# Optimization experiments

Measured on AMD Instinct MI355X. Metric: run time of the kernel, lower is better.

Reference implementation:

```python
import jax, jax.numpy as jnp
import numpy as np

NHEAD = 4
DIM = 256

def rotate_half(x):
    # interleaved: out[..., ::2] = -x[..., 1::2]; out[..., 1::2] = x[..., ::2]
    xe = x[..., ::2]
    xo = x[..., 1::2]
    return jnp.stack([-xo, xe], axis=-1).reshape(x.shape)

def rope_2d(q, k, H, W):
    Dh = q.shape[-1]
    half = Dh // 2
    inv_freq = 1.0 / (10000.0 ** (jnp.arange(half, dtype=jnp.float32) / half))  # [half]
    yy, xx = jnp.meshgrid(jnp.arange(H, dtype=jnp.float32), jnp.arange(W, dtype=jnp.float32), indexing='ij')
    ang_y = yy.reshape(-1)[:, None] * inv_freq  # [N, half]
    ang_x = xx.reshape(-1)[:, None] * inv_freq  # [N, half]
    cy, sy = jnp.cos(ang_y), jnp.sin(ang_y)
    cx, sx = jnp.cos(ang_x), jnp.sin(ang_x)
    def rot(t):
        t1 = t[..., :half]          # y-rotated half
        t2 = t[..., half:2 * half]  # x-rotated half
        ty = t1 * cy + rotate_half(t1) * sy
        tx = t2 * cx + rotate_half(t2) * sx
        return jnp.concatenate([ty, tx, t[..., 2 * half:]], axis=-1)
    return rot(q), rot(k)

def layernorm(x, g, b, eps=1e-5):
    mu = jnp.mean(x, axis=-1, keepdims=True)
    var = jnp.var(x, axis=-1, keepdims=True)
    return (x - mu) / jnp.sqrt(var + eps) * g + b

def setup_inputs() -> dict:
    key = jax.random.key(0)
    ks = jax.random.split(key, 8)
    B, Hs, Ws, C = 4, 48, 48, DIM
    N = Hs * Ws
    s = 0.02
    return {
        'x': jax.random.normal(ks[0], (B, N, C), dtype=jnp.float32),
        'Wqkv': jax.random.normal(ks[1], (3 * C, C), dtype=jnp.float32) * s,
        'Wproj': jax.random.normal(ks[2], (C, C), dtype=jnp.float32) * s,
        'g1': jnp.ones((C,), jnp.float32), 'b1': jnp.zeros((C,), jnp.float32),
        'g2': jnp.ones((C,), jnp.float32), 'b2': jnp.zeros((C,), jnp.float32),
        'W1': jax.random.normal(ks[3], (4 * C, C), dtype=jnp.float32) * s,
        'bf1': jnp.zeros((4 * C,), jnp.float32),
        'W2': jax.random.normal(ks[4], (C, 4 * C), dtype=jnp.float32) * s,
        'bf2': jnp.zeros((C,), jnp.float32),
        'H': Hs, 'W': Ws,
    }

def reference(x, Wqkv, Wproj, g1, b1, g2, b2, W1, bf1, W2, bf2, H, W):
    B, N, C = x.shape
    dh = C // NHEAD
    qkv = (x @ Wqkv.T).reshape(B, N, 3, NHEAD, dh).transpose(2, 0, 3, 1, 4)  # [3,B,h,N,dh]
    q, k, v = qkv[0], qkv[1], qkv[2]
    q, k = rope_2d(q, k, H, W)
    scores = jnp.einsum('bhnd,bhmd->bhnm', q, k) / jnp.sqrt(jnp.float32(dh))
    attn = jax.nn.softmax(scores, axis=-1)  # drop_attn is identity (p=0)
    out = jnp.einsum('bhnm,bhmd->bhnd', attn, v).transpose(0, 2, 1, 3).reshape(B, N, C)
    x = x + out @ Wproj.T
    x = layernorm(x, g1, b1)
    h = jax.nn.gelu(x @ W1.T + bf1, approximate=False)
    x = x + h @ W2.T + bf2
    return layernorm(x, g2, b2)
```

## Files before the change

### kernel.cpp

```cpp
#include <hip/hip_runtime.h>
#include <hip/hip_bf16.h>
#include <math.h>

typedef __hip_bfloat16 bf16;
typedef __attribute__((ext_vector_type(8))) short short8;
typedef __attribute__((ext_vector_type(4))) short short4v;
typedef __attribute__((ext_vector_type(4))) float f32x4;

#define NSEQ 2304
#define CDIM 256
#define NHD  4
#define DH   64

#if __has_builtin(__builtin_amdgcn_exp2f)
#define EXP2F __builtin_amdgcn_exp2f
#else
#define EXP2F exp2f
#endif

static __device__ __forceinline__ f32x4 mfma_bf16(short8 a, short8 b, f32x4 c) {
  return __builtin_amdgcn_mfma_f32_16x16x32_bf16(a, b, c, 0, 0, 0);
}
static __device__ __forceinline__ short8 ld8(const bf16* p) {
  return *reinterpret_cast<const short8*>(p);
}
static __device__ __forceinline__ short8 lds8(const bf16* p) {
  return *reinterpret_cast<const short8*>(p);
}
static __device__ __forceinline__ float b2f(short v) {
  unsigned int u = ((unsigned int)(unsigned short)v) << 16;
  return __uint_as_float(u);
}
static __device__ __forceinline__ short f2b(float f) {
  bf16 h = __float2bfloat16(f);
  return *reinterpret_cast<short*>(&h);
}

__global__ __launch_bounds__(256) void detect_kernel(const void* __restrict__ xraw,
                                                     int* __restrict__ flag) {
  int t = threadIdx.x;
  const unsigned short* s = (const unsigned short*)xraw;
  int bad = 0;
#pragma unroll
  for (int i = 0; i < 8; ++i) {
    unsigned idx = (((unsigned)(t * 8 + i)) * 9173u) & ((1u << 20) - 1);
    unsigned short v = s[idx * 2];
    unsigned e = (v >> 7) & 0xFFu;
    if (e > 133u) bad++;
  }
  __shared__ int tot;
  if (t == 0) tot = 0;
  __syncthreads();
  atomicAdd(&tot, bad);
  __syncthreads();
  if (t == 0) flag[0] = (tot >= 16) ? 1 : 0;
}

__global__ __launch_bounds__(256) void cvt_all_kernel(const void* sx, const void* sqkv, const void* sproj,
                                                      const void* sw1, const void* sw2,
                                                      const void* g1, const void* b1, const void* g2,
                                                      const void* b2, const void* bias1, const void* bias2,
                                                      bf16* dx, bf16* dqkv, bf16* dproj,
                                                      bf16* dw1, bf16* dw2, bf16* dsm,
                                                      const int* __restrict__ flag) {
  int is32 = flag[0];
  int bid = blockIdx.x;
  const void* src; bf16* dst; int i4;
  if (bid < 2304)      { src = sx;    dst = dx;    i4 = bid * 256 + threadIdx.x; }
  else if (bid < 2496) { src = sqkv;  dst = dqkv;  i4 = (bid - 2304) * 256 + threadIdx.x; }
  else if (bid < 2560) { src = sproj; dst = dproj; i4 = (bid - 2496) * 256 + threadIdx.x; }
  else if (bid < 2816) { src = sw1;   dst = dw1;   i4 = (bid - 2560) * 256 + threadIdx.x; }
  else if (bid < 3072) { src = sw2;   dst = dw2;   i4 = (bid - 2816) * 256 + threadIdx.x; }
  else {
    const void* srcs[6] = {g1, b1, g2, b2, bias1, bias2};
    const int ns[6] = {256, 256, 256, 256, 1024, 256};
    const int off[6] = {0, 256, 512, 768, 1024, 2048};
    int t = threadIdx.x;
#pragma unroll
    for (int j = 0; j < 6; ++j)
      for (int i = t; i < ns[j]; i += 256) {
        if (is32) dsm[off[j] + i] = __float2bfloat16(((const float*)srcs[j])[i]);
        else      dsm[off[j] + i] = ((const bf16*)srcs[j])[i];
      }
    return;
  }
  if (is32) {
    float4 v = ((const float4*)src)[i4];
    short4v o;
    o[0] = f2b(v.x); o[1] = f2b(v.y); o[2] = f2b(v.z); o[3] = f2b(v.w);
    ((short4v*)dst)[i4] = o;
  } else {
    ((short4v*)dst)[i4] = ((const short4v*)src)[i4];
  }
}

__global__ __launch_bounds__(256, 1) void qkv_kernel(const bf16* __restrict__ X,
                                                     const bf16* __restrict__ Wqkv,
                                                     bf16* __restrict__ Q, bf16* __restrict__ K,
                                                     bf16* __restrict__ Vt,
                                                     const int* __restrict__ Wp) {
  int wave = threadIdx.x >> 6, lane = threadIdx.x & 63;
  int l15 = lane & 15, quad = lane >> 4;
  int m0 = (blockIdx.x * 4 + wave) * 64;
  int n0 = blockIdx.y * 64;
  const bf16* arow = X + (size_t)(m0 + l15) * CDIM + quad * 8;
  const bf16* brow = Wqkv + (size_t)(n0 + l15) * CDIM + quad * 8;
  f32x4 z = {0.f, 0.f, 0.f, 0.f};
  f32x4 acc[4][4];
#pragma unroll
  for (int j = 0; j < 4; ++j)
#pragma unroll
    for (int i = 0; i < 4; ++i) acc[j][i] = z;

  short8 a[4], b[4];
#pragma unroll
  for (int i = 0; i < 4; ++i) a[i] = ld8(arow + (size_t)i * 16 * CDIM);
#pragma unroll
  for (int j = 0; j < 4; ++j) b[j] = ld8(brow + (size_t)j * 16 * CDIM);
#pragma unroll
  for (int kk = 32; kk <= CDIM; kk += 32) {
    short8 an[4], bn[4];
    if (kk < CDIM) {
#pragma unroll
      for (int i = 0; i < 4; ++i) an[i] = ld8(arow + (size_t)i * 16 * CDIM + kk);
#pragma unroll
      for (int j = 0; j < 4; ++j) bn[j] = ld8(brow + (size_t)j * 16 * CDIM + kk);
    }
#pragma unroll
    for (int j = 0; j < 4; ++j)
#pragma unroll
      for (int i = 0; i < 4; ++i) acc[j][i] = mfma_bf16(b[j], a[i], acc[j][i]);
    if (kk < CDIM) {
#pragma unroll
      for (int i = 0; i < 4; ++i) a[i] = an[i];
#pragma unroll
      for (int j = 0; j < 4; ++j) b[j] = bn[j];
    }
  }

  int which = n0 >> 8, h = (n0 & 255) >> 6;
  if (which == 2) {
#pragma unroll
    for (int j = 0; j < 4; ++j) {
      int d0 = j * 16 + quad * 4;
#pragma unroll
      for (int i = 0; i < 4; ++i) {
        int gm = m0 + i * 16 + l15;
        int bb = gm / NSEQ, n = gm % NSEQ;
        int bh = bb * NHD + h;
#pragma unroll
        for (int r = 0; r < 4; ++r)
          Vt[((size_t)bh * DH + d0 + r) * NSEQ + n] = __float2bfloat16(acc[j][i][r]);
      }
    }
  } else {
    int Wv = Wp[0];
    if (Wv <= 0 || Wv > 65536) Wv = 48;
    bf16* dst = (which == 0) ? Q : K;
    const float cc = -0.28782313662425574f;
    const float EC1 = 0.7498942434f, EC2 = 0.5623413252f, EC3 = 0.4216965034f;
#pragma unroll
    for (int i = 0; i < 4; ++i) {
      int gm = m0 + i * 16 + l15;
      int bb = gm / NSEQ, n = gm % NSEQ;
      int bh = bb * NHD + h;
      int py = n / Wv, px = n - py * Wv;
#pragma unroll
      for (int j = 0; j < 4; ++j) {
        int d0 = j * 16 + quad * 4;
        float pos = (d0 & 32) ? (float)px : (float)py;
        int base = d0 & 31;
        float fb = __expf(cc * (float)base);
        float f0 = fb, f1 = fb * EC1, f2 = fb * EC2, f3 = fb * EC3;
        float s0, c0, s1, c1, s2, c2, s3, c3;
        __sincosf(pos * f0, &s0, &c0);
        __sincosf(pos * f1, &s1, &c1);
        __sincosf(pos * f2, &s2, &c2);
        __sincosf(pos * f3, &s3, &c3);
        float a0 = acc[j][i][0], a1 = acc[j][i][1], a2 = acc[j][i][2], a3 = acc[j][i][3];
        short4v ov;
        ov[0] = f2b(a0 * c0 - a1 * s0);
        ov[1] = f2b(a1 * c1 + a0 * s1);
        ov[2] = f2b(a2 * c2 - a3 * s2);
        ov[3] = f2b(a3 * c3 + a2 * s3);
        *reinterpret_cast<short4v*>(dst + ((size_t)bh * NSEQ + n) * DH + d0) = ov;
      }
    }
  }
}

__global__ __launch_bounds__(128, 2) void attn_kernel(const bf16* __restrict__ Q, const bf16* __restrict__ K,
                                                      const bf16* __restrict__ Vt, bf16* __restrict__ AO) {
  int bh = blockIdx.x, qt = blockIdx.y;
  int tid = threadIdx.x;
  int wave = tid >> 6, lane = tid & 63;
  int l15 = lane & 15, quad = lane >> 4;
  int m0 = qt * 64 + wave * 32;
  const bf16* Qb = Q + (size_t)bh * NSEQ * DH;
  const bf16* Kb = K + (size_t)bh * NSEQ * DH;
  const bf16* Vb = Vt + (size_t)bh * DH * NSEQ;

  __shared__ __align__(16) bf16 kbuf[2][64 * 72];
  __shared__ __align__(16) bf16 vbuf[2][64 * 72];
  __shared__ __align__(16) bf16 plds[2][32 * 72];

  int rs[4], cs[4];
#pragma unroll
  for (int j = 0; j < 4; ++j) {
    int i = tid + j * 128;
    rs[j] = i >> 3;
    cs[j] = (i & 7) * 8;
  }

  const float QS = 0.18033688011112042f;
  short8 qa0 = ld8(Qb + (size_t)(m0 + l15) * DH + quad * 8);
  short8 qa1 = ld8(Qb + (size_t)(m0 + l15) * DH + 32 + quad * 8);
  short8 qb0 = ld8(Qb + (size_t)(m0 + 16 + l15) * DH + quad * 8);
  short8 qb1 = ld8(Qb + (size_t)(m0 + 16 + l15) * DH + 32 + quad * 8);
#pragma unroll
  for (int i = 0; i < 8; ++i) {
    qa0[i] = f2b(b2f(qa0[i]) * QS);
    qa1[i] = f2b(b2f(qa1[i]) * QS);
    qb0[i] = f2b(b2f(qb0[i]) * QS);
    qb1[i] = f2b(b2f(qb1[i]) * QS);
  }

  f32x4 z = {0.f, 0.f, 0.f, 0.f};
  f32x4 o[4] = {z, z, z, z};
  f32x4 o2[4] = {z, z, z, z};
  float l_run = 0.f, l_run2 = 0.f;
  bf16* pb = plds[wave];

#pragma unroll
  for (int j = 0; j < 4; ++j) {
    *reinterpret_cast<short8*>(kbuf[0] + rs[j] * 72 + cs[j]) = ld8(Kb + (size_t)rs[j] * DH + cs[j]);
    *reinterpret_cast<short8*>(vbuf[0] + rs[j] * 72 + cs[j]) = ld8(Vb + (size_t)rs[j] * NSEQ + cs[j]);
  }
  __syncthreads();

  for (int it = 0; it < NSEQ / 64; ++it) {
    int cur = it & 1;
    bool more = (it + 1 < NSEQ / 64);

    short8 kpre[4], vpre[4];
    if (more) {
      int kn = (it + 1) * 64;
#pragma unroll
      for (int j = 0; j < 4; ++j) {
        kpre[j] = ld8(Kb + (size_t)(kn + rs[j]) * DH + cs[j]);
        vpre[j] = ld8(Vb + (size_t)rs[j] * NSEQ + kn + cs[j]);
      }
    }

    const bf16* kb = kbuf[cur];
    const bf16* vb = vbuf[cur];

    f32x4 s[4], s2[4];
#pragma unroll
    for (int kt = 0; kt < 4; ++kt) {
      const bf16* kp = kb + (size_t)(kt * 16 + l15) * 72 + quad * 8;
      short8 kf0 = lds8(kp);
      short8 kf1 = lds8(kp + 32);
      s[kt] = mfma_bf16(kf0, qa0, z);
      s[kt] = mfma_bf16(kf1, qa1, s[kt]);
      s2[kt] = mfma_bf16(kf0, qb0, z);
      s2[kt] = mfma_bf16(kf1, qb1, s2[kt]);
    }

    float ls = 0.f, ls2 = 0.f;
#pragma unroll
    for (int kt = 0; kt < 4; ++kt) {
      float p0 = EXP2F(s[kt][0]);
      float p1 = EXP2F(s[kt][1]);
      float p2 = EXP2F(s[kt][2]);
      float p3 = EXP2F(s[kt][3]);
      ls += (p0 + p1) + (p2 + p3);
      short4v pk;
      pk[0] = f2b(p0); pk[1] = f2b(p1); pk[2] = f2b(p2); pk[3] = f2b(p3);
      *reinterpret_cast<short4v*>(pb + l15 * 72 + kt * 16 + quad * 4) = pk;
      float q0 = EXP2F(s2[kt][0]);
      float q1 = EXP2F(s2[kt][1]);
      float q2 = EXP2F(s2[kt][2]);
      float q3 = EXP2F(s2[kt][3]);
      ls2 += (q0 + q1) + (q2 + q3);
      short4v pk2;
      pk2[0] = f2b(q0); pk2[1] = f2b(q1); pk2[2] = f2b(q2); pk2[3] = f2b(q3);
      *reinterpret_cast<short4v*>(pb + (16 + l15) * 72 + kt * 16 + quad * 4) = pk2;
    }
    l_run += ls;
    l_run2 += ls2;

#pragma unroll
    for (int kt2 = 0; kt2 < 2; ++kt2) {
      short8 pfA = lds8(pb + l15 * 72 + kt2 * 32 + quad * 8);
      short8 pfB = lds8(pb + (16 + l15) * 72 + kt2 * 32 + quad * 8);
#pragma unroll
      for (int t = 0; t < 4; ++t) {
        short8 vf = lds8(vb + (size_t)(t * 16 + l15) * 72 + kt2 * 32 + quad * 8);
        o[t] = mfma_bf16(vf, pfA, o[t]);
        o2[t] = mfma_bf16(vf, pfB, o2[t]);
      }
    }

    if (more) {
      bf16* kn_ = kbuf[1 - cur];
      bf16* vn_ = vbuf[1 - cur];
#pragma unroll
      for (int j = 0; j < 4; ++j) {
        *reinterpret_cast<short8*>(kn_ + rs[j] * 72 + cs[j]) = kpre[j];
        *reinterpret_cast<short8*>(vn_ + rs[j] * 72 + cs[j]) = vpre[j];
      }
    }
    __syncthreads();
  }

  l_run += __shfl_xor(l_run, 16);
  l_run += __shfl_xor(l_run, 32);
  l_run2 += __shfl_xor(l_run2, 16);
  l_run2 += __shfl_xor(l_run2, 32);
  float inv = 1.f / l_run;
  float inv2 = 1.f / l_run2;
  int b = bh >> 2, h = bh & 3;
  bf16* orow = AO + ((size_t)b * NSEQ + (m0 + l15)) * CDIM + h * DH;
  bf16* orow2 = AO + ((size_t)b * NSEQ + (m0 + 16 + l15)) * CDIM + h * DH;
#pragma unroll
  for (int t = 0; t < 4; ++t) {
    short4v ov, ov2;
#pragma unroll
    for (int r = 0; r < 4; ++r) {
      ov[r] = f2b(o[t][r] * inv);
      ov2[r] = f2b(o2[t][r] * inv2);
    }
    *reinterpret_cast<short4v*>(orow + t * 16 + quad * 4) = ov;
    *reinterpret_cast<short4v*>(orow2 + t * 16 + quad * 4) = ov2;
  }
}

template <int KD, int EPI, int TI>
__global__ __launch_bounds__(256) void gemm128(const bf16* __restrict__ A, const bf16* __restrict__ Wm,
                                               const bf16* __restrict__ bias, const bf16* __restrict__ res,
                                               bf16* __restrict__ outp, int NC) {
  constexpr int KS = KD / 32;
  constexpr int AR = TI * 32;
  int tid = threadIdx.x;
  int wave = tid >> 6, lane = tid & 63;
  int l15 = lane & 15, quad = lane >> 4;
  int wm = (wave >> 1) * (TI * 16);
  int wn = (wave & 1) * 64;
  int m0 = blockIdx.x * AR;
  int n0 = blockIdx.y * 128;

  __shared__ __align__(16) bf16 abuf[2][AR * 40];
  __shared__ __align__(16) bf16 bbuf[2][128 * 40];

  int sr = tid >> 2, sc = (tid & 3) * 8;

  const bf16* ag[TI / 2];
#pragma unroll
  for (int u = 0; u < TI / 2; ++u) ag[u] = A + (size_t)(m0 + sr + u * 64) * KD + sc;
  const bf16* bg0 = Wm + (size_t)(n0 + sr) * KD + sc;
  const bf16* bg1 = Wm + (size_t)(n0 + 64 + sr) * KD + sc;

  f32x4 z = {0.f, 0.f, 0.f, 0.f};
  f32x4 acc[4][TI];
#pragma unroll
  for (int j = 0; j < 4; ++j)
#pragma unroll
    for (int i = 0; i < TI; ++i) acc[j][i] = z;

#pragma unroll
  for (int u = 0; u < TI / 2; ++u)
    *reinterpret_cast<short8*>(abuf[0] + (sr + u * 64) * 40 + sc) = ld8(ag[u]);
  *reinterpret_cast<short8*>(bbuf[0] + sr * 40 + sc) = ld8(bg0);
  *reinterpret_cast<short8*>(bbuf[0] + (64 + sr) * 40 + sc) = ld8(bg1);
  __syncthreads();

  for (int s = 0; s < KS; ++s) {
    int cur = s & 1;
    bool more = (s + 1 < KS);
    short8 anx[TI / 2], bnx0, bnx1;
    if (more) {
#pragma unroll
      for (int u = 0; u < TI / 2; ++u) anx[u] = ld8(ag[u] + (s + 1) * 32);
      bnx0 = ld8(bg0 + (s + 1) * 32);
      bnx1 = ld8(bg1 + (s + 1) * 32);
    }
    short8 af[TI], bf_[4];
#pragma unroll
    for (int i = 0; i < TI; ++i)
      af[i] = lds8(abuf[cur] + (size_t)(wm + i * 16 + l15) * 40 + quad * 8);
#pragma unroll
    for (int j = 0; j < 4; ++j)
      bf_[j] = lds8(bbuf[cur] + (size_t)(wn + j * 16 + l15) * 40 + quad * 8);
#pragma unroll
    for (int j = 0; j < 4; ++j)
#pragma unroll
      for (int i = 0; i < TI; ++i)
        acc[j][i] = mfma_bf16(bf_[j], af[i], acc[j][i]);
    if (more) {
#pragma unroll
      for (int u = 0; u < TI / 2; ++u)
        *reinterpret_cast<short8*>(abuf[1 - cur] + (sr + u * 64) * 40 + sc) = anx[u];
      *reinterpret_cast<short8*>(bbuf[1 - cur] + sr * 40 + sc) = bnx0;
      *reinterpret_cast<short8*>(bbuf[1 - cur] + (64 + sr) * 40 + sc) = bnx1;
    }
    __syncthreads();
  }

#pragma unroll
  for (int j = 0; j < 4; ++j) {
    int col0 = n0 + wn + j * 16 + quad * 4;
    float bb4[4];
    if (EPI != 0) {
      short4v bl = *reinterpret_cast<const short4v*>(bias + col0);
#pragma unroll
      for (int r = 0; r < 4; ++r) bb4[r] = b2f(bl[r]);
    }
#pragma unroll
    for (int i = 0; i < TI; ++i) {
      size_t idx = (size_t)(m0 + wm + i * 16 + l15) * NC + col0;
      short4v ov;
      if (EPI == 0) {
        short4v rl = *reinterpret_cast<const short4v*>(res + idx);
#pragma unroll
        for (int r = 0; r < 4; ++r) ov[r] = f2b(acc[j][i][r] + b2f(rl[r]));
      } else if (EPI == 1) {
#pragma unroll
        for (int r = 0; r < 4; ++r) {
          float hv = acc[j][i][r] + bb4[r];
          ov[r] = f2b(0.5f * hv * (1.f + erff(hv * 0.70710678118f)));
        }
      } else {
        short4v rl = *reinterpret_cast<const short4v*>(res + idx);
#pragma unroll
        for (int r = 0; r < 4; ++r) ov[r] = f2b(acc[j][i][r] + bb4[r] + b2f(rl[r]));
      }
      *reinterpret_cast<short4v*>(outp + idx) = ov;
    }
  }
}

__global__ __launch_bounds__(256) void ln_kernel(const bf16* __restrict__ X, const bf16* __restrict__ g,
                                                 const bf16* __restrict__ bv, bf16* __restrict__ out) {
  int row = blockIdx.x * 4 + (threadIdx.x >> 6);
  int lane = threadIdx.x & 63;
  short4v raw = *reinterpret_cast<const short4v*>(X + (size_t)row * CDIM + lane * 4);
  float vv[4];
  float s = 0.f, sq = 0.f;
#pragma unroll
  for (int i = 0; i < 4; ++i) {
    float f = b2f(raw[i]);
    vv[i] = f; s += f; sq += f * f;
  }
#pragma unroll
  for (int off = 1; off < 64; off <<= 1) { s += __shfl_xor(s, off); sq += __shfl_xor(sq, off); }
  float mu = s * (1.f / CDIM);
  float var = sq * (1.f / CDIM) - mu * mu;
  float rstd = rsqrtf(var + 1e-5f);
#pragma unroll
  for (int i = 0; i < 4; ++i) {
    int c = lane * 4 + i;
    out[(size_t)row * CDIM + c] =
        __float2bfloat16((vv[i] - mu) * rstd * __bfloat162float(g[c]) + __bfloat162float(bv[c]));
  }
}

__global__ __launch_bounds__(256) void ln_out_kernel(const bf16* __restrict__ X, const bf16* __restrict__ g,
                                                     const bf16* __restrict__ bv, void* __restrict__ out,
                                                     const int* __restrict__ flag) {
  int is32 = flag[0];
  int row = blockIdx.x * 4 + (threadIdx.x >> 6);
  int lane = threadIdx.x & 63;
  short4v raw = *reinterpret_cast<const short4v*>(X + (size_t)row * CDIM + lane * 4);
  float vv[4];
  float s = 0.f, sq = 0.f;
#pragma unroll
  for (int i = 0; i < 4; ++i) {
    float f = b2f(raw[i]);
    vv[i] = f; s += f; sq += f * f;
  }
#pragma unroll
  for (int off = 1; off < 64; off <<= 1) { s += __shfl_xor(s, off); sq += __shfl_xor(sq, off); }
  float mu = s * (1.f / CDIM);
  float var = sq * (1.f / CDIM) - mu * mu;
  float rstd = rsqrtf(var + 1e-5f);
#pragma unroll
  for (int i = 0; i < 4; ++i) {
    int c = lane * 4 + i;
    size_t idx = (size_t)row * CDIM + c;
    float v = (vv[i] - mu) * rstd * __bfloat162float(g[c]) + __bfloat162float(bv[c]);
    if (is32) ((float*)out)[idx] = v;
    else      ((bf16*)out)[idx] = __float2bfloat16(v);
  }
}

extern "C" void kernel_launch(void* const* d_in, const int* in_sizes, int n_in,
                              void* d_out, int out_size, void* d_ws, size_t ws_size,
                              hipStream_t stream) {
  const int* Wp = (const int*)d_in[12];

  char* ws = (char*)d_ws;
  const size_t SZ = 4718592;
  bf16* Qc  = (bf16*)(ws + 0 * SZ);
  bf16* Kc  = (bf16*)(ws + 1 * SZ);
  bf16* Vt  = (bf16*)(ws + 2 * SZ);
  bf16* AO  = (bf16*)(ws + 3 * SZ);
  bf16* F   = (bf16*)(ws + 4 * SZ);
  bf16* Y   = (bf16*)(ws + 5 * SZ);
  bf16* xc  = (bf16*)(ws + 6 * SZ);
  bf16* G   = (bf16*)(ws + 0);
  bf16* Wqkvc  = (bf16*)(ws + 7 * SZ);
  bf16* Wprojc = (bf16*)(ws + 7 * SZ + 393216);
  bf16* W1c    = (bf16*)(ws + 7 * SZ + 524288);
  bf16* W2c    = (bf16*)(ws + 7 * SZ + 1048576);
  bf16* smallc = (bf16*)(ws + 7 * SZ + 1572864);
  bf16* g1c  = smallc + 0;
  bf16* b1c  = smallc + 256;
  bf16* g2c  = smallc + 512;
  bf16* b2c  = smallc + 768;
  bf16* bf1c = smallc + 1024;
  bf16* bf2c = smallc + 2048;
  int*  flagp = (int*)(ws + 7 * SZ + 1581568);
  bf16* outsc = (bf16*)d_out;

  detect_kernel<<<1, 256, 0, stream>>>(d_in[0], flagp);
  cvt_all_kernel<<<3073, 256, 0, stream>>>(d_in[0], d_in[1], d_in[2], d_in[7], d_in[9],
                                           d_in[3], d_in[4], d_in[5], d_in[6], d_in[8], d_in[10],
                                           xc, Wqkvc, Wprojc, W1c, W2c, smallc, flagp);

  qkv_kernel<<<dim3(36, 12), 256, 0, stream>>>(xc, Wqkvc, Qc, Kc, Vt, Wp);
  attn_kernel<<<dim3(16, 36), 128, 0, stream>>>(Qc, Kc, Vt, AO);
  gemm128<256, 0, 2><<<dim3(144, 2), 256, 0, stream>>>(AO, Wprojc, nullptr, xc, outsc, 256);
  ln_kernel<<<2304, 256, 0, stream>>>(outsc, g1c, b1c, F);
  gemm128<256, 1, 4><<<dim3(72, 8), 256, 0, stream>>>(F, W1c, bf1c, nullptr, G, 1024);
  gemm128<1024, 2, 2><<<dim3(144, 2), 256, 0, stream>>>(G, W2c, bf2c, F, Y, 256);
  ln_out_kernel<<<2304, 256, 0, stream>>>(Y, g2c, b2c, d_out, flagp);
}
```

Baseline: 217.7 us.

## Split attention key tiles across two wave pairs with LDS reduction

The attention block grows from 2 to 4 waves. Each pair of waves takes half of every 64-key tile, which halves per-wave MFMA and exp work per iteration. Partial outputs and row sums are combined through LDS, reusing the K buffer, at the end. This raises wave-level parallelism for the 576 blocks at the cost of an extra reduction step and more threads contending at each barrier.

Result: faster. 212.4 us (-2.5%).

```diff
diff --git a/kernel.cpp b/kernel.cpp
--- a/kernel.cpp
+++ b/kernel.cpp
@@ -189,28 +189,25 @@
   }
 }
 
-__global__ __launch_bounds__(128, 2) void attn_kernel(const bf16* __restrict__ Q, const bf16* __restrict__ K,
+__global__ __launch_bounds__(256, 3) void attn_kernel(const bf16* __restrict__ Q, const bf16* __restrict__ K,
                                                       const bf16* __restrict__ Vt, bf16* __restrict__ AO) {
   int bh = blockIdx.x, qt = blockIdx.y;
   int tid = threadIdx.x;
   int wave = tid >> 6, lane = tid & 63;
   int l15 = lane & 15, quad = lane >> 4;
-  int m0 = qt * 64 + wave * 32;
+  int qf = wave & 1;
+  int ks = wave >> 1;
+  int m0 = qt * 64 + qf * 32;
   const bf16* Qb = Q + (size_t)bh * NSEQ * DH;
   const bf16* Kb = K + (size_t)bh * NSEQ * DH;
   const bf16* Vb = Vt + (size_t)bh * DH * NSEQ;
 
   __shared__ __align__(16) bf16 kbuf[2][64 * 72];
   __shared__ __align__(16) bf16 vbuf[2][64 * 72];
-  __shared__ __align__(16) bf16 plds[2][32 * 72];
-
-  int rs[4], cs[4];
-#pragma unroll
-  for (int j = 0; j < 4; ++j) {
-    int i = tid + j * 128;
-    rs[j] = i >> 3;
-    cs[j] = (i & 7) * 8;
-  }
+  __shared__ __align__(16) bf16 plds[4][32 * 40];
+
+  int r1 = tid >> 3, c1 = (tid & 7) * 8;
+  int r1b = r1 + 32;
 
   const float QS = 0.18033688011112042f;
   short8 qa0 = ld8(Qb + (size_t)(m0 + l15) * DH + quad * 8);
@@ -231,34 +228,32 @@
   float l_run = 0.f, l_run2 = 0.f;
   bf16* pb = plds[wave];
 
-#pragma unroll
-  for (int j = 0; j < 4; ++j) {
-    *reinterpret_cast<short8*>(kbuf[0] + rs[j] * 72 + cs[j]) = ld8(Kb + (size_t)rs[j] * DH + cs[j]);
-    *reinterpret_cast<short8*>(vbuf[0] + rs[j] * 72 + cs[j]) = ld8(Vb + (size_t)rs[j] * NSEQ + cs[j]);
-  }
+  *reinterpret_cast<short8*>(kbuf[0] + r1 * 72 + c1)  = ld8(Kb + (size_t)r1 * DH + c1);
+  *reinterpret_cast<short8*>(kbuf[0] + r1b * 72 + c1) = ld8(Kb + (size_t)r1b * DH + c1);
+  *reinterpret_cast<short8*>(vbuf[0] + r1 * 72 + c1)  = ld8(Vb + (size_t)r1 * NSEQ + c1);
+  *reinterpret_cast<short8*>(vbuf[0] + r1b * 72 + c1) = ld8(Vb + (size_t)r1b * NSEQ + c1);
   __syncthreads();
 
   for (int it = 0; it < NSEQ / 64; ++it) {
     int cur = it & 1;
     bool more = (it + 1 < NSEQ / 64);
 
-    short8 kpre[4], vpre[4];
+    short8 kpA, kpB, vpA, vpB;
     if (more) {
       int kn = (it + 1) * 64;
-#pragma unroll
-      for (int j = 0; j < 4; ++j) {
-        kpre[j] = ld8(Kb + (size_t)(kn + rs[j]) * DH + cs[j]);
-        vpre[j] = ld8(Vb + (size_t)rs[j] * NSEQ + kn + cs[j]);
-      }
+      kpA = ld8(Kb + (size_t)(kn + r1) * DH + c1);
+      kpB = ld8(Kb + (size_t)(kn + r1b) * DH + c1);
+      vpA = ld8(Vb + (size_t)r1 * NSEQ + kn + c1);
+      vpB = ld8(Vb + (size_t)r1b * NSEQ + kn + c1);
     }
 
     const bf16* kb = kbuf[cur];
     const bf16* vb = vbuf[cur];
 
-    f32x4 s[4], s2[4];
-#pragma unroll
-    for (int kt = 0; kt < 4; ++kt) {
-      const bf16* kp = kb + (size_t)(kt * 16 + l15) * 72 + quad * 8;
+    f32x4 s[2], s2[2];
+#pragma unroll
+    for (int kt = 0; kt < 2; ++kt) {
+      const bf16* kp = kb + (size_t)(ks * 32 + kt * 16 + l15) * 72 + quad * 8;
       short8 kf0 = lds8(kp);
       short8 kf1 = lds8(kp + 32);
       s[kt] = mfma_bf16(kf0, qa0, z);
@@ -269,7 +264,7 @@
 
     float ls = 0.f, ls2 = 0.f;
 #pragma unroll
-    for (int kt = 0; kt < 4; ++kt) {
+    for (int kt = 0; kt < 2; ++kt) {
       float p0 = EXP2F(s[kt][0]);
       float p1 = EXP2F(s[kt][1]);
       float p2 = EXP2F(s[kt][2]);
@@ -277,7 +272,7 @@
       ls += (p0 + p1) + (p2 + p3);
       short4v pk;
       pk[0] = f2b(p0); pk[1] = f2b(p1); pk[2] = f2b(p2); pk[3] = f2b(p3);
-      *reinterpret_cast<short4v*>(pb + l15 * 72 + kt * 16 + quad * 4) = pk;
+      *reinterpret_cast<short4v*>(pb + l15 * 40 + kt * 16 + quad * 4) = pk;
       float q0 = EXP2F(s2[kt][0]);
       float q1 = EXP2F(s2[kt][1]);
       float q2 = EXP2F(s2[kt][2]);
@@ -285,18 +280,17 @@
       ls2 += (q0 + q1) + (q2 + q3);
       short4v pk2;
       pk2[0] = f2b(q0); pk2[1] = f2b(q1); pk2[2] = f2b(q2); pk2[3] = f2b(q3);
-      *reinterpret_cast<short4v*>(pb + (16 + l15) * 72 + kt * 16 + quad * 4) = pk2;
+      *reinterpret_cast<short4v*>(pb + (16 + l15) * 40 + kt * 16 + quad * 4) = pk2;
     }
     l_run += ls;
     l_run2 += ls2;
 
-#pragma unroll
-    for (int kt2 = 0; kt2 < 2; ++kt2) {
-      short8 pfA = lds8(pb + l15 * 72 + kt2 * 32 + quad * 8);
-      short8 pfB = lds8(pb + (16 + l15) * 72 + kt2 * 32 + quad * 8);
+    {
+      short8 pfA = lds8(pb + l15 * 40 + quad * 8);
+      short8 pfB = lds8(pb + (16 + l15) * 40 + quad * 8);
 #pragma unroll
       for (int t = 0; t < 4; ++t) {
-        short8 vf = lds8(vb + (size_t)(t * 16 + l15) * 72 + kt2 * 32 + quad * 8);
+        short8 vf = lds8(vb + (size_t)(t * 16 + l15) * 72 + ks * 32 + quad * 8);
         o[t] = mfma_bf16(vf, pfA, o[t]);
         o2[t] = mfma_bf16(vf, pfB, o2[t]);
       }
@@ -305,34 +299,62 @@
     if (more) {
       bf16* kn_ = kbuf[1 - cur];
       bf16* vn_ = vbuf[1 - cur];
-#pragma unroll
-      for (int j = 0; j < 4; ++j) {
-        *reinterpret_cast<short8*>(kn_ + rs[j] * 72 + cs[j]) = kpre[j];
-        *reinterpret_cast<short8*>(vn_ + rs[j] * 72 + cs[j]) = vpre[j];
-      }
+      *reinterpret_cast<short8*>(kn_ + r1 * 72 + c1)  = kpA;
+      *reinterpret_cast<short8*>(kn_ + r1b * 72 + c1) = kpB;
+      *reinterpret_cast<short8*>(vn_ + r1 * 72 + c1)  = vpA;
+      *reinterpret_cast<short8*>(vn_ + r1b * 72 + c1) = vpB;
     }
     __syncthreads();
   }
 
-  l_run += __shfl_xor(l_run, 16);
-  l_run += __shfl_xor(l_run, 32);
-  l_run2 += __shfl_xor(l_run2, 16);
-  l_run2 += __shfl_xor(l_run2, 32);
-  float inv = 1.f / l_run;
-  float inv2 = 1.f / l_run2;
-  int b = bh >> 2, h = bh & 3;
-  bf16* orow = AO + ((size_t)b * NSEQ + (m0 + l15)) * CDIM + h * DH;
-  bf16* orow2 = AO + ((size_t)b * NSEQ + (m0 + 16 + l15)) * CDIM + h * DH;
-#pragma unroll
-  for (int t = 0; t < 4; ++t) {
-    short4v ov, ov2;
-#pragma unroll
-    for (int r = 0; r < 4; ++r) {
-      ov[r] = f2b(o[t][r] * inv);
-      ov2[r] = f2b(o2[t][r] * inv2);
-    }
-    *reinterpret_cast<short4v*>(orow + t * 16 + quad * 4) = ov;
-    *reinterpret_cast<short4v*>(orow2 + t * 16 + quad * 4) = ov2;
+  float* scr = (float*)kbuf;
+  int slot = qf * 64 + lane;
+  if (ks == 1) {
+    float* p = scr + slot * 36;
+#pragma unroll
+    for (int t = 0; t < 4; ++t) {
+      *reinterpret_cast<f32x4*>(p + t * 4) = o[t];
+      *reinterpret_cast<f32x4*>(p + 16 + t * 4) = o2[t];
+    }
+    p[32] = l_run;
+    p[33] = l_run2;
+  }
+  __syncthreads();
+  if (ks == 0) {
+    float* p = scr + slot * 36;
+#pragma unroll
+    for (int t = 0; t < 4; ++t) {
+      f32x4 pa = *reinterpret_cast<f32x4*>(p + t * 4);
+      f32x4 pb2 = *reinterpret_cast<f32x4*>(p + 16 + t * 4);
+#pragma unroll
+      for (int r = 0; r < 4; ++r) {
+        o[t][r] += pa[r];
+        o2[t][r] += pb2[r];
+      }
+    }
+    l_run += p[32];
+    l_run2 += p[33];
+
+    l_run += __shfl_xor(l_run, 16);
+    l_run += __shfl_xor(l_run, 32);
+    l_run2 += __shfl_xor(l_run2, 16);
+    l_run2 += __shfl_xor(l_run2, 32);
+    float inv = 1.f / l_run;
+    float inv2 = 1.f / l_run2;
+    int b = bh >> 2, h = bh & 3;
+    bf16* orow = AO + ((size_t)b * NSEQ + (m0 + l15)) * CDIM + h * DH;
+    bf16* orow2 = AO + ((size_t)b * NSEQ + (m0 + 16 + l15)) * CDIM + h * DH;
+#pragma unroll
+    for (int t = 0; t < 4; ++t) {
+      short4v ov, ov2;
+#pragma unroll
+      for (int r = 0; r < 4; ++r) {
+        ov[r] = f2b(o[t][r] * inv);
+        ov2[r] = f2b(o2[t][r] * inv2);
+      }
+      *reinterpret_cast<short4v*>(orow + t * 16 + quad * 4) = ov;
+      *reinterpret_cast<short4v*>(orow2 + t * 16 + quad * 4) = ov2;
+    }
   }
 }
 
@@ -529,7 +551,7 @@
                                            xc, Wqkvc, Wprojc, W1c, W2c, smallc, flagp);
 
   qkv_kernel<<<dim3(36, 12), 256, 0, stream>>>(xc, Wqkvc, Qc, Kc, Vt, Wp);
-  attn_kernel<<<dim3(16, 36), 128, 0, stream>>>(Qc, Kc, Vt, AO);
+  attn_kernel<<<dim3(16, 36), 256, 0, stream>>>(Qc, Kc, Vt, AO);
   gemm128<256, 0, 2><<<dim3(144, 2), 256, 0, stream>>>(AO, Wprojc, nullptr, xc, outsc, 256);
   ln_kernel<<<2304, 256, 0, stream>>>(outsc, g1c, b1c, F);
   gemm128<256, 1, 4><<<dim3(72, 8), 256, 0, stream>>>(F, W1c, bf1c, nullptr, G, 1024);
```
